# Kernel tuning notes

Measured on AMD Instinct MI355X. Metric: run time of the kernel, lower is better.

## Reference

```python
import jax, jax.numpy as jnp
import numpy as np

B, PD, CD = 8192, 1024, 1024


def setup_inputs() -> dict:
    key = jax.random.key(0)
    ks = jax.random.split(key, 10)
    u = lambda k, shape: jax.random.uniform(k, shape, dtype=jnp.float32, minval=-0.05, maxval=0.05)
    return {
        "P": jax.random.normal(ks[0], (B, PD), dtype=jnp.float32),
        "C1": jax.random.normal(ks[1], (B, CD), dtype=jnp.float32),
        "C2": jax.random.normal(ks[2], (B, CD), dtype=jnp.float32),
        "C3": jax.random.normal(ks[3], (B, CD), dtype=jnp.float32),
        "C4": jax.random.normal(ks[4], (B, CD), dtype=jnp.float32),
        "GateWeight_P": u(ks[5], (PD, CD)),
        "GateWeight_C": u(ks[6], (CD, CD)),
        "GateBias": u(ks[7], (CD,)),
        "OutWeight": u(ks[8], (PD, CD)),
        "OutBias": u(ks[9], (CD, 1)),
    }


def reference(P, C1, C2, C3, C4, GateWeight_P, GateWeight_C, GateBias, OutWeight, OutBias):
    # Stack the 4 choice branches: [4, B, C]
    Cs = jnp.stack([C1, C2, C3, C4], axis=0)
    WP = P @ GateWeight_P                                  # [B, C]
    WC = jnp.einsum("kbc,cd->kbd", Cs, GateWeight_C)       # [4, B, C]
    g = jax.nn.sigmoid(WP[None] + WC + GateBias)           # [4, B, C]
    C_dash = Cs * g                                        # [4, B, C]
    WP_out = P @ OutWeight                                 # [B, C]
    scores = jnp.einsum("kbc,bc->kb", C_dash, WP_out)      # batch_dot axes=[1,1]
    bias = jnp.einsum("kbc,c->kb", C_dash, OutBias[:, 0])  # K.dot(C_dash, OutBias)
    return (scores + bias).T                               # [B, 4]
```

## Files before the change

kernel.cpp:

```cpp
#include <hip/hip_runtime.h>
#include <hip/hip_bf16.h>


#define B_  8192
#define PD_ 1024
#define CD_ 1024

typedef unsigned short ushort_t;
typedef __attribute__((ext_vector_type(8))) short    short8;
typedef __attribute__((ext_vector_type(8))) unsigned short ushort8;
typedef __attribute__((ext_vector_type(4))) float    floatx4;

__device__ __forceinline__ float bf2f(unsigned short u) {
    return __uint_as_float(((unsigned)u) << 16);
}
__device__ __forceinline__ unsigned short f2bf(float f) {
    unsigned u = __float_as_uint(f);
    unsigned r = u + 0x7FFFu + ((u >> 16) & 1u);
    return (unsigned short)(r >> 16);
}

__global__ __launch_bounds__(256) void cast_kernel(const float* __restrict__ src,
                                                   ushort_t* __restrict__ dst, int n4) {
    int i = blockIdx.x * 256 + threadIdx.x;
    if (i >= n4) return;
    float4 v = ((const float4*)src)[i];
    ushort4 o;
    o.x = f2bf(v.x); o.y = f2bf(v.y); o.z = f2bf(v.z); o.w = f2bf(v.w);
    ((ushort4*)dst)[i] = o;
}

__global__ __launch_bounds__(256) void transpose_cast(const float* __restrict__ src,
                                                      ushort_t* __restrict__ dst,
                                                      int R, int C) {
    __shared__ float tile[32][33];
    int c0 = blockIdx.x * 32, r0 = blockIdx.y * 32;
    int x = threadIdx.x, y = threadIdx.y;
    for (int i = y; i < 32; i += 8)
        tile[i][x] = src[(size_t)(r0 + i) * C + c0 + x];
    __syncthreads();
    for (int i = y; i < 32; i += 8)
        dst[(size_t)(c0 + i) * R + r0 + x] = f2bf(tile[x][i]);
}

__device__ __forceinline__ void gl_lds16(const void* g, void* l) {
    __builtin_amdgcn_global_load_lds((const __attribute__((address_space(1))) void*)g,
                                     (__attribute__((address_space(3))) void*)l, 16, 0, 0);
}

__global__ __launch_bounds__(256) void gemm_bt(const ushort_t* __restrict__ A,
                                               const ushort_t* __restrict__ Bt,
                                               ushort_t* __restrict__ C,
                                               int M, int N, int K) {
    __shared__ ushort_t lA[128 * 32];
    __shared__ ushort_t lB[128 * 32];
    const int t    = threadIdx.x;
    const int wave = t >> 6, lane = t & 63;
    const int quad = lane >> 4, l16 = lane & 15;
    const int wm   = wave >> 1, wn  = wave & 1;
    const int tileM = blockIdx.y * 128, tileN = blockIdx.x * 128;

    const int ch0 = wave * 2;
    const int sr0 = ch0 * 16 + (lane >> 2);
    const int sc  = (lane & 3) * 8;
    const int lo0 = ch0 * 512 + lane * 8;

    const ushort_t* Ag0 = A  + (size_t)(tileM + sr0)      * K + sc;
    const ushort_t* Ag1 = A  + (size_t)(tileM + sr0 + 16) * K + sc;
    const ushort_t* Bg0 = Bt + (size_t)(tileN + sr0)      * K + sc;
    const ushort_t* Bg1 = Bt + (size_t)(tileN + sr0 + 16) * K + sc;

    floatx4 acc[4][4];
#pragma unroll
    for (int i = 0; i < 4; i++)
#pragma unroll
        for (int j = 0; j < 4; j++) acc[i][j] = (floatx4)0.f;

    for (int k0 = 0; k0 < K; k0 += 32) {
        gl_lds16(Ag0 + k0, &lA[lo0]);
        gl_lds16(Ag1 + k0, &lA[lo0 + 512]);
        gl_lds16(Bg0 + k0, &lB[lo0]);
        gl_lds16(Bg1 + k0, &lB[lo0 + 512]);
        __syncthreads();

        short8 af[4], bfr[4];
#pragma unroll
        for (int mi = 0; mi < 4; mi++)
            af[mi] = *(const short8*)&lA[(wm * 64 + mi * 16 + l16) * 32 + quad * 8];
#pragma unroll
        for (int ni = 0; ni < 4; ni++)
            bfr[ni] = *(const short8*)&lB[(wn * 64 + ni * 16 + l16) * 32 + quad * 8];
#pragma unroll
        for (int mi = 0; mi < 4; mi++)
#pragma unroll
            for (int ni = 0; ni < 4; ni++)
                acc[mi][ni] = __builtin_amdgcn_mfma_f32_16x16x32_bf16(
                    af[mi], bfr[ni], acc[mi][ni], 0, 0, 0);
        __syncthreads();
    }

#pragma unroll
    for (int mi = 0; mi < 4; mi++)
#pragma unroll
        for (int ni = 0; ni < 4; ni++)
#pragma unroll
            for (int r = 0; r < 4; r++) {
                int row = tileM + wm * 64 + mi * 16 + quad * 4 + r;
                int col = tileN + wn * 64 + ni * 16 + l16;
                C[(size_t)row * N + col] = f2bf(acc[mi][ni][r]);
            }
}

__global__ __launch_bounds__(256) void epilogue(const ushort_t* __restrict__ WPcat,
                                                const ushort_t* __restrict__ WC,
                                                const ushort_t* __restrict__ Call,
                                                const float* __restrict__ Gb,
                                                const float* __restrict__ Ob,
                                                float* __restrict__ out) {
    const int wave = threadIdx.x >> 6, lane = threadIdx.x & 63;
    const int b = blockIdx.x * 4 + wave;
    float acc[4] = {0.f, 0.f, 0.f, 0.f};

#pragma unroll
    for (int it = 0; it < 2; it++) {
        const int c = it * 512 + lane * 8;
        ushort8 wp  = *(const ushort8*)&WPcat[(size_t)b * 2048 + c];
        ushort8 wpo = *(const ushort8*)&WPcat[(size_t)b * 2048 + 1024 + c];
        floatx4 g0 = *(const floatx4*)&Gb[c];
        floatx4 g1 = *(const floatx4*)&Gb[c + 4];
        floatx4 o0 = *(const floatx4*)&Ob[c];
        floatx4 o1 = *(const floatx4*)&Ob[c + 4];
        float gb[8], ob[8];
#pragma unroll
        for (int j = 0; j < 4; j++) { gb[j] = g0[j]; gb[4 + j] = g1[j]; ob[j] = o0[j]; ob[4 + j] = o1[j]; }

        float po[8], wpf[8];
#pragma unroll
        for (int j = 0; j < 8; j++) {
            wpf[j] = bf2f(wp[j]);
            po[j]  = bf2f(wpo[j]) + ob[j];
        }
#pragma unroll
        for (int k = 0; k < 4; k++) {
            size_t off = ((size_t)k * B_ + b) * 1024 + c;
            ushort8 cv = *(const ushort8*)&Call[off];
            ushort8 wc = *(const ushort8*)&WC[off];
            float s = 0.f;
#pragma unroll
            for (int j = 0; j < 8; j++) {
                float x = wpf[j] + bf2f(wc[j]) + gb[j];
                float g = 1.f / (1.f + __expf(-x));
                s += bf2f(cv[j]) * g * po[j];
            }
            acc[k] += s;
        }
    }
#pragma unroll
    for (int k = 0; k < 4; k++) {
#pragma unroll
        for (int off = 32; off > 0; off >>= 1)
            acc[k] += __shfl_down(acc[k], off);
    }
    if (lane == 0) {
        out[(size_t)b * 4 + 0] = acc[0];
        out[(size_t)b * 4 + 1] = acc[1];
        out[(size_t)b * 4 + 2] = acc[2];
        out[(size_t)b * 4 + 3] = acc[3];
    }
}

extern "C" void kernel_launch(void* const* d_in, const int* in_sizes, int n_in,
                              void* d_out, int out_size, void* d_ws, size_t ws_size,
                              hipStream_t stream) {
    (void)in_sizes; (void)n_in; (void)out_size; (void)ws_size;
    const float* P   = (const float*)d_in[0];
    const float* C1  = (const float*)d_in[1];
    const float* C2  = (const float*)d_in[2];
    const float* C3  = (const float*)d_in[3];
    const float* C4  = (const float*)d_in[4];
    const float* GWP = (const float*)d_in[5];
    const float* GWC = (const float*)d_in[6];
    const float* Gb  = (const float*)d_in[7];
    const float* OW  = (const float*)d_in[8];
    const float* Ob  = (const float*)d_in[9];
    float* out = (float*)d_out;

    char* ws = (char*)d_ws;
    ushort_t* Pb    = (ushort_t*)(ws);
    ushort_t* Call  = (ushort_t*)(ws + (16u  << 20));
    ushort_t* Wcat  = (ushort_t*)(ws + (80u  << 20));
    ushort_t* GWCt  = (ushort_t*)(ws + (84u  << 20));
    ushort_t* WPcat = (ushort_t*)(ws + (86u  << 20));
    ushort_t* WC    = (ushort_t*)(ws + (118u << 20));

    const int n4 = B_ * PD_ / 4;
    const int cgrid = n4 / 256;

    cast_kernel<<<cgrid, 256, 0, stream>>>(P,  Pb, n4);
    cast_kernel<<<cgrid, 256, 0, stream>>>(C1, Call + (size_t)0 * B_ * CD_, n4);
    cast_kernel<<<cgrid, 256, 0, stream>>>(C2, Call + (size_t)1 * B_ * CD_, n4);
    cast_kernel<<<cgrid, 256, 0, stream>>>(C3, Call + (size_t)2 * B_ * CD_, n4);
    cast_kernel<<<cgrid, 256, 0, stream>>>(C4, Call + (size_t)3 * B_ * CD_, n4);

    transpose_cast<<<dim3(32, 32), dim3(32, 8), 0, stream>>>(GWP, Wcat,               1024, 1024);
    transpose_cast<<<dim3(32, 32), dim3(32, 8), 0, stream>>>(OW,  Wcat + 1024 * 1024, 1024, 1024);
    transpose_cast<<<dim3(32, 32), dim3(32, 8), 0, stream>>>(GWC, GWCt,               1024, 1024);

    gemm_bt<<<dim3(16, 64), 256, 0, stream>>>(Pb, Wcat, WPcat, B_, 2048, 1024);
    gemm_bt<<<dim3(8, 256), 256, 0, stream>>>(Call, GWCt, WC, 4 * B_, 1024, 1024);

    epilogue<<<B_ / 4, 256, 0, stream>>>(WPcat, WC, Call, Gb, Ob, out);
}
```

Baseline: 409.0 us.

## Batch cast/transpose/GEMM launches and XOR-swizzle GEMM LDS layout

Merges the five cast launches into one kernel, the three weight transposes into one 3D-grid launch, and the two GEMMs into a single grouped launch that picks its problem from the block index. It also XOR-swizzles the K-chunk column when staging tiles into LDS, and swizzles the fragment reads to match, to reduce LDS bank conflicts on the MFMA operand loads. The aim is fewer launches and tail gaps plus cheaper LDS reads. The cost is extra branching and index arithmetic, and the swizzle must stay consistent between the async global-to-LDS stores and the fragment reads.

```diff
diff --git a/kernel.cpp b/kernel.cpp
--- a/kernel.cpp
+++ b/kernel.cpp
@@ -20,20 +20,44 @@
     return (unsigned short)(r >> 16);
 }
 
-__global__ __launch_bounds__(256) void cast_kernel(const float* __restrict__ src,
-                                                   ushort_t* __restrict__ dst, int n4) {
-    int i = blockIdx.x * 256 + threadIdx.x;
-    if (i >= n4) return;
+__global__ __launch_bounds__(256) void cast5_kernel(const float* __restrict__ P,
+                                                    const float* __restrict__ C1,
+                                                    const float* __restrict__ C2,
+                                                    const float* __restrict__ C3,
+                                                    const float* __restrict__ C4,
+                                                    ushort_t* __restrict__ Pb,
+                                                    ushort_t* __restrict__ Call) {
+    const int seg = blockIdx.x >> 13;
+    const int i   = (blockIdx.x & 8191) * 256 + threadIdx.x;
+    const float* src;
+    ushort_t* dst;
+    switch (seg) {
+        case 0: src = P;  dst = Pb; break;
+        case 1: src = C1; dst = Call; break;
+        case 2: src = C2; dst = Call + (size_t)1 * B_ * CD_; break;
+        case 3: src = C3; dst = Call + (size_t)2 * B_ * CD_; break;
+        default: src = C4; dst = Call + (size_t)3 * B_ * CD_; break;
+    }
     float4 v = ((const float4*)src)[i];
     ushort4 o;
     o.x = f2bf(v.x); o.y = f2bf(v.y); o.z = f2bf(v.z); o.w = f2bf(v.w);
     ((ushort4*)dst)[i] = o;
 }
 
-__global__ __launch_bounds__(256) void transpose_cast(const float* __restrict__ src,
-                                                      ushort_t* __restrict__ dst,
-                                                      int R, int C) {
+__global__ __launch_bounds__(256) void transpose3(const float* __restrict__ GWP,
+                                                  const float* __restrict__ OW,
+                                                  const float* __restrict__ GWC,
+                                                  ushort_t* __restrict__ Wcat,
+                                                  ushort_t* __restrict__ GWCt) {
     __shared__ float tile[32][33];
+    const float* src;
+    ushort_t* dst;
+    switch (blockIdx.z) {
+        case 0: src = GWP; dst = Wcat; break;
+        case 1: src = OW;  dst = Wcat + 1024 * 1024; break;
+        default: src = GWC; dst = GWCt; break;
+    }
+    const int R = 1024, C = 1024;
     int c0 = blockIdx.x * 32, r0 = blockIdx.y * 32;
     int x = threadIdx.x, y = threadIdx.y;
     for (int i = y; i < 32; i += 8)
@@ -48,27 +72,46 @@
                                      (__attribute__((address_space(3))) void*)l, 16, 0, 0);
 }
 
-__global__ __launch_bounds__(256) void gemm_bt(const ushort_t* __restrict__ A,
-                                               const ushort_t* __restrict__ Bt,
-                                               ushort_t* __restrict__ C,
-                                               int M, int N, int K) {
+__global__ __launch_bounds__(256) void gemm_fused(const ushort_t* __restrict__ Pb,
+                                                  const ushort_t* __restrict__ Wcat,
+                                                  ushort_t* __restrict__ WPcat,
+                                                  const ushort_t* __restrict__ Call,
+                                                  const ushort_t* __restrict__ GWCt,
+                                                  ushort_t* __restrict__ WC) {
     __shared__ ushort_t lA[128 * 32];
     __shared__ ushort_t lB[128 * 32];
+    const int K = 1024;
+
+    const ushort_t *A, *Bt;
+    ushort_t* Cc;
+    int N, tileM, tileN;
+    const int bid = blockIdx.x;
+    if (bid < 1024) {
+        A = Pb; Bt = Wcat; Cc = WPcat; N = 2048;
+        tileN = (bid & 15) * 128; tileM = (bid >> 4) * 128;
+    } else {
+        const int b2 = bid - 1024;
+        A = Call; Bt = GWCt; Cc = WC; N = 1024;
+        tileN = (b2 & 7) * 128; tileM = (b2 >> 3) * 128;
+    }
+
     const int t    = threadIdx.x;
     const int wave = t >> 6, lane = t & 63;
     const int quad = lane >> 4, l16 = lane & 15;
     const int wm   = wave >> 1, wn  = wave & 1;
-    const int tileM = blockIdx.y * 128, tileN = blockIdx.x * 128;
-
-    const int ch0 = wave * 2;
-    const int sr0 = ch0 * 16 + (lane >> 2);
-    const int sc  = (lane & 3) * 8;
-    const int lo0 = ch0 * 512 + lane * 8;
-
-    const ushort_t* Ag0 = A  + (size_t)(tileM + sr0)      * K + sc;
-    const ushort_t* Ag1 = A  + (size_t)(tileM + sr0 + 16) * K + sc;
-    const ushort_t* Bg0 = Bt + (size_t)(tileN + sr0)      * K + sc;
-    const ushort_t* Bg1 = Bt + (size_t)(tileN + sr0 + 16) * K + sc;
+
+    const int ch0  = wave * 2;
+    const int srow = lane >> 2;
+    const int skc  = (lane & 3) ^ ((lane >> 4) & 3);
+    const int sc   = skc * 8;
+    const int lo0  = ch0 * 512 + lane * 8;
+
+    const ushort_t* Ag0 = A  + (size_t)(tileM + ch0 * 16 + srow)      * K + sc;
+    const ushort_t* Ag1 = A  + (size_t)(tileM + ch0 * 16 + srow + 16) * K + sc;
+    const ushort_t* Bg0 = Bt + (size_t)(tileN + ch0 * 16 + srow)      * K + sc;
+    const ushort_t* Bg1 = Bt + (size_t)(tileN + ch0 * 16 + srow + 16) * K + sc;
+
+    const int fro = (l16 * 4 + (quad ^ (l16 >> 2))) * 8;
 
     floatx4 acc[4][4];
 #pragma unroll
@@ -86,10 +129,10 @@
         short8 af[4], bfr[4];
 #pragma unroll
         for (int mi = 0; mi < 4; mi++)
-            af[mi] = *(const short8*)&lA[(wm * 64 + mi * 16 + l16) * 32 + quad * 8];
+            af[mi] = *(const short8*)&lA[(wm * 4 + mi) * 512 + fro];
 #pragma unroll
         for (int ni = 0; ni < 4; ni++)
-            bfr[ni] = *(const short8*)&lB[(wn * 64 + ni * 16 + l16) * 32 + quad * 8];
+            bfr[ni] = *(const short8*)&lB[(wn * 4 + ni) * 512 + fro];
 #pragma unroll
         for (int mi = 0; mi < 4; mi++)
 #pragma unroll
@@ -107,7 +150,7 @@
             for (int r = 0; r < 4; r++) {
                 int row = tileM + wm * 64 + mi * 16 + quad * 4 + r;
                 int col = tileN + wn * 64 + ni * 16 + l16;
-                C[(size_t)row * N + col] = f2bf(acc[mi][ni][r]);
+                Cc[(size_t)row * N + col] = f2bf(acc[mi][ni][r]);
             }
 }
 
@@ -193,21 +236,10 @@
     ushort_t* WPcat = (ushort_t*)(ws + (86u  << 20));
     ushort_t* WC    = (ushort_t*)(ws + (118u << 20));
 
-    const int n4 = B_ * PD_ / 4;
-    const int cgrid = n4 / 256;
-
-    cast_kernel<<<cgrid, 256, 0, stream>>>(P,  Pb, n4);
-    cast_kernel<<<cgrid, 256, 0, stream>>>(C1, Call + (size_t)0 * B_ * CD_, n4);
-    cast_kernel<<<cgrid, 256, 0, stream>>>(C2, Call + (size_t)1 * B_ * CD_, n4);
-    cast_kernel<<<cgrid, 256, 0, stream>>>(C3, Call + (size_t)2 * B_ * CD_, n4);
-    cast_kernel<<<cgrid, 256, 0, stream>>>(C4, Call + (size_t)3 * B_ * CD_, n4);
-
-    transpose_cast<<<dim3(32, 32), dim3(32, 8), 0, stream>>>(GWP, Wcat,               1024, 1024);
-    transpose_cast<<<dim3(32, 32), dim3(32, 8), 0, stream>>>(OW,  Wcat + 1024 * 1024, 1024, 1024);
-    transpose_cast<<<dim3(32, 32), dim3(32, 8), 0, stream>>>(GWC, GWCt,               1024, 1024);
-
-    gemm_bt<<<dim3(16, 64), 256, 0, stream>>>(Pb, Wcat, WPcat, B_, 2048, 1024);
-    gemm_bt<<<dim3(8, 256), 256, 0, stream>>>(Call, GWCt, WC, 4 * B_, 1024, 1024);
+    cast5_kernel<<<5 * 8192, 256, 0, stream>>>(P, C1, C2, C3, C4, Pb, Call);
+    transpose3<<<dim3(32, 32, 3), dim3(32, 8), 0, stream>>>(GWP, OW, GWC, Wcat, GWCt);
+
+    gemm_fused<<<3072, 256, 0, stream>>>(Pb, Wcat, WPcat, Call, GWCt, WC);
 
     epilogue<<<B_ / 4, 256, 0, stream>>>(WPcat, WC, Call, Gb, Ob, out);
 }
```

Result: faster. 361.6 us (-11.6%).
